# Kernel optimization log

Measured on AMD Instinct MI355X. Metric: run time of the kernel, lower is better.

The kernel has to match this reference:

```python
import jax, jax.numpy as jnp
import numpy as np

ALPHA = 0.2  # LeakyReLU negative slope
MASK_FILL = -9e15


def setup_inputs() -> dict:
    key = jax.random.key(0)
    k_x, k_adj, k_W, k_a = jax.random.split(key, 4)
    B, N, Fin, T, O = 8, 1024, 64, 8, 128
    x = jax.random.normal(k_x, (B, N, Fin, T), dtype=jnp.float32)
    adj = (jax.random.uniform(k_adj, (N, N)) < 0.05).astype(jnp.float32)
    adj = jnp.maximum(adj, jnp.eye(N, dtype=jnp.float32))
    W = jax.random.normal(k_W, (Fin, O), dtype=jnp.float32) * (1.414 * (6.0 / (Fin + O)) ** 0.5)
    a = jax.random.normal(k_a, (2 * O, 1), dtype=jnp.float32) * (1.414 * (6.0 / (2 * O + 1)) ** 0.5)
    return {"x": x, "adj": adj, "W": W, "a": a}


def reference(x, adj, W, a):
    # x: (B, N, Fin, T), adj: (N, N), W: (Fin, O), a: (2O, 1)
    O = W.shape[1]
    xt = jnp.transpose(x, (0, 3, 1, 2))                 # (B, T, N, Fin)
    Wh = jnp.einsum('btnf,fo->btno', xt, W)             # (B, T, N, O)
    a1 = a[:O, 0]                                       # (O,)
    a2 = a[O:, 0]                                       # (O,)
    Wh1 = Wh @ a1                                       # (B, T, N)
    Wh2 = Wh @ a2                                       # (B, T, N)
    e = Wh1[..., :, None] + Wh2[..., None, :]           # (B, T, N, N): e_ij = Wh1_i + Wh2_j
    e = jax.nn.leaky_relu(e, negative_slope=ALPHA)
    e = jnp.where(adj > 0, e, MASK_FILL)
    attn = jax.nn.softmax(e, axis=-1)                   # softmax over neighbors j (torch dim=1 on (N,N))
    # dropout on attention is identity at inference (training=False)
    h_prime = jnp.einsum('btij,btjo->btio', attn, Wh)   # (B, T, N, O)
    out = jnp.transpose(h_prime, (0, 2, 3, 1))          # (B, N, O, T)
    return jax.nn.elu(out)                              # concat=True -> ELU
```

## Files before the change

kernel.cpp:

```cpp
#include <hip/hip_runtime.h>
#include <math.h>
#include <stdint.h>

#define ALPHA 0.2f

typedef __attribute__((ext_vector_type(8)))  short bf16x8;
typedef __attribute__((ext_vector_type(4)))  float f32x4;
typedef __attribute__((ext_vector_type(16))) float f32x16;

__device__ __forceinline__ uint32_t pack_bf16(float a, float b) {
    return ((__float_as_uint(a) + 0x8000u) >> 16) |
           ((__float_as_uint(b) + 0x8000u) & 0xFFFF0000u);
}

__global__ __launch_bounds__(512) void k_wh(const float* __restrict__ x,
                                            const float* __restrict__ W,
                                            const float* __restrict__ a,
                                            uint4* __restrict__ Whf,
                                            float* __restrict__ Wh1,
                                            float* __restrict__ Wh2) {
    __shared__ float xs[16 * 512];
    __shared__ float Wv[128 * 68];

    const int tid = threadIdx.x;
    const int b   = blockIdx.x & 7;
    const int jt  = blockIdx.x >> 3;

    const float4* xg4 = (const float4*)(x + (size_t)(b * 1024 + jt * 16) * 512);
    #pragma unroll
    for (int i = 0; i < 4; ++i) {
        int    idx = tid + i * 512;
        float4 v   = xg4[idx];
        int jl  = idx >> 7;
        int rem = idx & 127;
        int f   = rem >> 1;
        int tq  = rem & 1;
        int kk  = f ^ ((jl >> 2) << 2);
        float* dst = &xs[jl * 512 + (tq * 4) * 64 + kk];
        dst[0]   = v.x;
        dst[64]  = v.y;
        dst[128] = v.z;
        dst[192] = v.w;
    }
    const float4* Wg4 = (const float4*)W;
    #pragma unroll
    for (int i = 0; i < 4; ++i) {
        int    idx = tid + i * 512;
        float4 v   = Wg4[idx];
        int k  = idx >> 5;
        int o0 = (idx & 31) * 4;
        #pragma unroll
        for (int c = 0; c < 4; ++c) {
            int o   = o0 + c;
            int adr = o * 68 + ((((k >> 2) ^ ((o >> 3) & 7)) << 2) | (k & 3));
            Wv[adr] = (&v.x)[c];
        }
    }
    __syncthreads();

    const int w  = tid >> 6;
    const int l  = tid & 63;
    const int q  = l >> 4;
    const int om = l & 15;
    const int t  = w;

    float acc[4][8];
    #pragma unroll
    for (int jj = 0; jj < 4; ++jj)
        #pragma unroll
        for (int nt = 0; nt < 8; ++nt) acc[jj][nt] = 0.f;

    for (int kc = 0; kc < 64; kc += 4) {
        float4 xv[4], wv[8];
        const int kx = kc ^ (q << 2);
        #pragma unroll
        for (int jj = 0; jj < 4; ++jj)
            xv[jj] = *(const float4*)&xs[(q * 4 + jj) * 512 + t * 64 + kx];
        #pragma unroll
        for (int nt = 0; nt < 8; ++nt) {
            int og  = nt * 16 + om;
            int grp = (kc >> 2) ^ ((nt * 2 + (om >> 3)) & 7);
            wv[nt]  = *(const float4*)&Wv[og * 68 + grp * 4];
        }
        #pragma unroll
        for (int jj = 0; jj < 4; ++jj) {
            #pragma unroll
            for (int nt = 0; nt < 8; ++nt) {
                float s = acc[jj][nt];
                s = fmaf(xv[jj].x, wv[nt].x, s);
                s = fmaf(xv[jj].y, wv[nt].y, s);
                s = fmaf(xv[jj].z, wv[nt].z, s);
                s = fmaf(xv[jj].w, wv[nt].w, s);
                acc[jj][nt] = s;
            }
        }
    }

    const int bt = b * 8 + t;

    float a1v[8], a2v[8];
    #pragma unroll
    for (int nt = 0; nt < 8; ++nt) {
        a1v[nt] = a[nt * 16 + om];
        a2v[nt] = a[128 + nt * 16 + om];
    }
    #pragma unroll
    for (int jj = 0; jj < 4; ++jj) {
        float s1 = 0.f, s2 = 0.f;
        #pragma unroll
        for (int nt = 0; nt < 8; ++nt) {
            s1 = fmaf(acc[jj][nt], a1v[nt], s1);
            s2 = fmaf(acc[jj][nt], a2v[nt], s2);
        }
        #pragma unroll
        for (int off = 1; off < 16; off <<= 1) {
            s1 += __shfl_xor(s1, off);
            s2 += __shfl_xor(s2, off);
        }
        if (om == 0) {
            int j = jt * 16 + q * 4 + jj;
            Wh1[bt * 1024 + j] = s1;
            Wh2[bt * 1024 + j] = s2;
        }
    }

    #pragma unroll
    for (int nt = 0; nt < 8; ++nt) {
        uint2 st;
        st.x = pack_bf16(acc[0][nt], acc[1][nt]);
        st.y = pack_bf16(acc[2][nt], acc[3][nt]);
        int    lane2 = ((q >> 1) << 5) | ((nt & 1) << 4) | om;
        size_t fidx  = ((size_t)(bt * 4 + (nt >> 1)) * 64 + jt) * 64 + lane2;
        char*  p     = (char*)(Whf + fidx) + ((q & 1) << 3);
        *(uint2*)p = st;
    }
}

__global__ __launch_bounds__(256) void k_adjb(const float* __restrict__ adj,
                                              unsigned char* __restrict__ adjq) {
    int idx = blockIdx.x * 256 + threadIdx.x;
    int i   = idx >> 7;
    int pos = idx & 127;
    const float4* a4 = (const float4*)adj + idx * 2;
    float4 v0 = a4[0], v1 = a4[1];
    unsigned int by = 0;
    by |= (v0.x > 0.f) ? 1u : 0u;
    by |= (v0.y > 0.f) ? 2u : 0u;
    by |= (v0.z > 0.f) ? 4u : 0u;
    by |= (v0.w > 0.f) ? 8u : 0u;
    by |= (v1.x > 0.f) ? 16u : 0u;
    by |= (v1.y > 0.f) ? 32u : 0u;
    by |= (v1.z > 0.f) ? 64u : 0u;
    by |= (v1.w > 0.f) ? 128u : 0u;
    adjq[(i << 7) + ((pos & 1) << 6) + (((pos >> 1) & 1) << 5) + (pos >> 2)] = (unsigned char)by;
}

__global__ __launch_bounds__(256) void k_agg(const uint4* __restrict__ Whf,
                                             const float* __restrict__ Wh1,
                                             const float* __restrict__ Wh2,
                                             const unsigned char* __restrict__ adjq,
                                             float* __restrict__ out) {
    __shared__ __attribute__((aligned(16))) uint4 bstage[2][2048];
    __shared__ __attribute__((aligned(16))) float efsE[1024];
    __shared__ __attribute__((aligned(16))) float efsF[1024];
    __shared__ float wh1s[128];
    __shared__ float m2s[4];

    const int tid   = threadIdx.x;
    const int b     = blockIdx.x & 7;
    const int t     = (blockIdx.x >> 3) & 7;
    const int itile = blockIdx.x >> 6;
    const int bt    = b * 8 + t;
    const int i0    = itile * 128;

    const int w   = tid >> 6;
    const int l   = tid & 63;
    const int col = l & 31;
    const int g   = l >> 5;
    const int row = w * 32 + col;

    const uint4* plane = Whf + (size_t)bt * 16384;

    uint4 pf[8];
    #pragma unroll
    for (int f = 0; f < 8; ++f) pf[f] = plane[(w * 64 + f) * 64 + l];

    const uint4* ap = (const uint4*)(adjq + ((size_t)(i0 + row) << 7) + (g << 6));
    uint4 am[4];
    #pragma unroll
    for (int f = 0; f < 4; ++f) am[f] = ap[f];

    const float* wh2g = Wh2 + bt * 1024;
    float mx = -1e30f;
    #pragma unroll
    for (int rep = 0; rep < 4; ++rep) {
        int   j  = tid + rep * 256;
        float h2 = wh2g[j];
        efsE[j] = __expf(h2);
        efsF[j] = __expf(ALPHA * h2);
        mx = fmaxf(mx, h2);
    }
    #pragma unroll
    for (int off = 1; off < 64; off <<= 1) mx = fmaxf(mx, __shfl_xor(mx, off));
    if (l == 0) m2s[w] = mx;
    if (tid < 128) wh1s[tid] = Wh1[bt * 1024 + i0 + tid];

    #pragma unroll
    for (int f = 0; f < 8; ++f) bstage[0][(w * 8 + f) * 64 + l] = pf[f];
    __syncthreads();

    const float M2 = fmaxf(fmaxf(m2s[0], m2s[1]), fmaxf(m2s[2], m2s[3]));
    const float h1 = wh1s[row];
    const float e0 = h1 + M2;
    const float mp = fmaxf(e0, ALPHA * e0);
    const float Af = __expf(h1 - mp);
    const float Bf = __expf(ALPHA * h1 - mp);

    f32x16 acc[4];
    #pragma unroll
    for (int nt2 = 0; nt2 < 4; ++nt2)
        #pragma unroll
        for (int r = 0; r < 16; ++r) acc[nt2][r] = 0.f;
    f32x16 accl;
    #pragma unroll
    for (int r = 0; r < 16; ++r) accl[r] = 0.f;

    bf16x8 ones;
    #pragma unroll
    for (int i = 0; i < 8; ++i) ones[i] = (short)0x3F80;

    #pragma unroll
    for (int u = 0; u < 8; ++u) {
        if (u + 1 < 8) {
            #pragma unroll
            for (int f = 0; f < 8; ++f)
                pf[f] = plane[(w * 64 + (u + 1) * 8 + f) * 64 + l];
        }

        #pragma unroll
        for (int ts = 0; ts < 8; ++ts) {
            const int jb = u * 128 + ts * 16 + g * 8;
            float4 E0 = *(const float4*)&efsE[jb];
            float4 E1 = *(const float4*)&efsE[jb + 4];
            float4 F0 = *(const float4*)&efsF[jb];
            float4 F1 = *(const float4*)&efsF[jb + 4];

            const int      pe = (ts & 1) * 32 + u * 4 + (ts >> 1);
            const uint4    av = am[pe >> 4];
            const int      cc = (pe >> 2) & 3;
            const uint32_t cw = (cc == 0) ? av.x : (cc == 1) ? av.y
                               : (cc == 2) ? av.z : av.w;
            const uint32_t by = (cw >> ((pe & 3) * 8)) & 0xFFu;

            float p[8];
            p[0] = fmaxf(Af * E0.x, Bf * F0.x) * (float)((by >> 0) & 1u);
            p[1] = fmaxf(Af * E0.y, Bf * F0.y) * (float)((by >> 1) & 1u);
            p[2] = fmaxf(Af * E0.z, Bf * F0.z) * (float)((by >> 2) & 1u);
            p[3] = fmaxf(Af * E0.w, Bf * F0.w) * (float)((by >> 3) & 1u);
            p[4] = fmaxf(Af * E1.x, Bf * F1.x) * (float)((by >> 4) & 1u);
            p[5] = fmaxf(Af * E1.y, Bf * F1.y) * (float)((by >> 5) & 1u);
            p[6] = fmaxf(Af * E1.z, Bf * F1.z) * (float)((by >> 6) & 1u);
            p[7] = fmaxf(Af * E1.w, Bf * F1.w) * (float)((by >> 7) & 1u);

            union { uint32_t u32[4]; bf16x8 v; } pk;
            #pragma unroll
            for (int r = 0; r < 4; ++r)
                pk.u32[r] = pack_bf16(p[2 * r], p[2 * r + 1]);

            #pragma unroll
            for (int nt2 = 0; nt2 < 4; ++nt2) {
                union { uint4 u4; bf16x8 v; } br;
                br.u4 = bstage[u & 1][(nt2 * 8 + ts) * 64 + l];
                acc[nt2] = __builtin_amdgcn_mfma_f32_32x32x16_bf16(
                    pk.v, br.v, acc[nt2], 0, 0, 0);
            }
            accl = __builtin_amdgcn_mfma_f32_32x32x16_bf16(
                pk.v, ones, accl, 0, 0, 0);
        }

        if (u + 1 < 8) {
            #pragma unroll
            for (int f = 0; f < 8; ++f)
                bstage[(u + 1) & 1][(w * 8 + f) * 64 + l] = pf[f];
        }
        __syncthreads();
    }

    float* og = out + ((size_t)(b * 1024 + i0 + w * 32)) * 1024 + t;
    #pragma unroll
    for (int reg = 0; reg < 16; ++reg) {
        const int   r    = (reg & 3) + 8 * (reg >> 2) + 4 * g;
        const float linv = 1.0f / accl[reg];
        #pragma unroll
        for (int nt2 = 0; nt2 < 4; ++nt2) {
            float v = acc[nt2][reg] * linv;
            v = v > 0.f ? v : __expf(v) - 1.f;
            og[(size_t)r * 1024 + (nt2 * 32 + col) * 8] = v;
        }
    }
}

extern "C" void kernel_launch(void* const* d_in, const int* in_sizes, int n_in,
                              void* d_out, int out_size, void* d_ws, size_t ws_size,
                              hipStream_t stream) {
    const float* x   = (const float*)d_in[0];
    const float* adj = (const float*)d_in[1];
    const float* W   = (const float*)d_in[2];
    const float* a   = (const float*)d_in[3];
    float* out = (float*)d_out;

    uint4*         Whf  = (uint4*)d_ws;
    float*         Wh1  = (float*)(Whf + 1048576);
    float*         Wh2  = Wh1 + 65536;
    unsigned char* adjq = (unsigned char*)(Wh2 + 65536);

    k_wh  <<<512, 512, 0, stream>>>(x, W, a, Whf, Wh1, Wh2);
    k_adjb<<<512, 256, 0, stream>>>(adj, adjq);
    k_agg <<<512, 256, 0, stream>>>(Whf, Wh1, Wh2, adjq, out);
}
```

Measured before the change: 145.4 us.

## Merge preprocessing kernels, async LDS staging, scalar row-sum, MFMA priority

The adjacency bit-packing kernel is folded into the Wh projection kernel as extra blocks, which saves one launch. In the aggregation kernel, Wh tiles are copied global-to-LDS with global_load_lds instead of passing through registers. The softmax denominator is now a per-thread scalar sum plus a shuffle rather than an extra MFMA against a ones vector. s_setprio is raised around the MFMA block. Risks: the double-buffered async LDS writes may need explicit vmcnt waits before the barrier. The row sum now uses fp32 p values while the numerator uses bf16-rounded ones, a small numeric mismatch.

```diff
diff --git a/kernel.cpp b/kernel.cpp
--- a/kernel.cpp
+++ b/kernel.cpp
@@ -5,7 +5,6 @@
 #define ALPHA 0.2f
 
 typedef __attribute__((ext_vector_type(8)))  short bf16x8;
-typedef __attribute__((ext_vector_type(4)))  float f32x4;
 typedef __attribute__((ext_vector_type(16))) float f32x16;
 
 __device__ __forceinline__ uint32_t pack_bf16(float a, float b) {
@@ -13,14 +12,43 @@
            ((__float_as_uint(b) + 0x8000u) & 0xFFFF0000u);
 }
 
-__global__ __launch_bounds__(512) void k_wh(const float* __restrict__ x,
-                                            const float* __restrict__ W,
-                                            const float* __restrict__ a,
-                                            uint4* __restrict__ Whf,
-                                            float* __restrict__ Wh1,
-                                            float* __restrict__ Wh2) {
+__device__ __forceinline__ void gload_lds16(const uint4* g, uint4* l) {
+    __builtin_amdgcn_global_load_lds(
+        (const __attribute__((address_space(1))) void*)g,
+        (__attribute__((address_space(3))) void*)l,
+        16, 0, 0);
+}
+
+__global__ __launch_bounds__(512) void k_pre(const float* __restrict__ x,
+                                             const float* __restrict__ W,
+                                             const float* __restrict__ a,
+                                             const float* __restrict__ adj,
+                                             uint4* __restrict__ Whf,
+                                             float* __restrict__ Wh1,
+                                             float* __restrict__ Wh2,
+                                             unsigned char* __restrict__ adjq) {
     __shared__ float xs[16 * 512];
     __shared__ float Wv[128 * 68];
+
+    if (blockIdx.x >= 512) {
+        int idx = (blockIdx.x - 512) * 512 + threadIdx.x;
+        int i   = idx >> 7;
+        int pos = idx & 127;
+        const float4* a4 = (const float4*)adj + idx * 2;
+        float4 v0 = a4[0], v1 = a4[1];
+        unsigned int by = 0;
+        by |= (v0.x > 0.f) ? 1u : 0u;
+        by |= (v0.y > 0.f) ? 2u : 0u;
+        by |= (v0.z > 0.f) ? 4u : 0u;
+        by |= (v0.w > 0.f) ? 8u : 0u;
+        by |= (v1.x > 0.f) ? 16u : 0u;
+        by |= (v1.y > 0.f) ? 32u : 0u;
+        by |= (v1.z > 0.f) ? 64u : 0u;
+        by |= (v1.w > 0.f) ? 128u : 0u;
+        adjq[(i << 7) + ((pos & 1) << 6) + (((pos >> 1) & 1) << 5) + (pos >> 2)] =
+            (unsigned char)by;
+        return;
+    }
 
     const int tid = threadIdx.x;
     const int b   = blockIdx.x & 7;
@@ -136,25 +164,6 @@
     }
 }
 
-__global__ __launch_bounds__(256) void k_adjb(const float* __restrict__ adj,
-                                              unsigned char* __restrict__ adjq) {
-    int idx = blockIdx.x * 256 + threadIdx.x;
-    int i   = idx >> 7;
-    int pos = idx & 127;
-    const float4* a4 = (const float4*)adj + idx * 2;
-    float4 v0 = a4[0], v1 = a4[1];
-    unsigned int by = 0;
-    by |= (v0.x > 0.f) ? 1u : 0u;
-    by |= (v0.y > 0.f) ? 2u : 0u;
-    by |= (v0.z > 0.f) ? 4u : 0u;
-    by |= (v0.w > 0.f) ? 8u : 0u;
-    by |= (v1.x > 0.f) ? 16u : 0u;
-    by |= (v1.y > 0.f) ? 32u : 0u;
-    by |= (v1.z > 0.f) ? 64u : 0u;
-    by |= (v1.w > 0.f) ? 128u : 0u;
-    adjq[(i << 7) + ((pos & 1) << 6) + (((pos >> 1) & 1) << 5) + (pos >> 2)] = (unsigned char)by;
-}
-
 __global__ __launch_bounds__(256) void k_agg(const uint4* __restrict__ Whf,
                                              const float* __restrict__ Wh1,
                                              const float* __restrict__ Wh2,
@@ -181,9 +190,9 @@
 
     const uint4* plane = Whf + (size_t)bt * 16384;
 
-    uint4 pf[8];
-    #pragma unroll
-    for (int f = 0; f < 8; ++f) pf[f] = plane[(w * 64 + f) * 64 + l];
+    #pragma unroll
+    for (int f = 0; f < 8; ++f)
+        gload_lds16(&plane[(w * 64 + f) * 64 + l], &bstage[0][(w * 8 + f) * 64]);
 
     const uint4* ap = (const uint4*)(adjq + ((size_t)(i0 + row) << 7) + (g << 6));
     uint4 am[4];
@@ -204,9 +213,6 @@
     for (int off = 1; off < 64; off <<= 1) mx = fmaxf(mx, __shfl_xor(mx, off));
     if (l == 0) m2s[w] = mx;
     if (tid < 128) wh1s[tid] = Wh1[bt * 1024 + i0 + tid];
-
-    #pragma unroll
-    for (int f = 0; f < 8; ++f) bstage[0][(w * 8 + f) * 64 + l] = pf[f];
     __syncthreads();
 
     const float M2 = fmaxf(fmaxf(m2s[0], m2s[1]), fmaxf(m2s[2], m2s[3]));
@@ -221,20 +227,15 @@
     for (int nt2 = 0; nt2 < 4; ++nt2)
         #pragma unroll
         for (int r = 0; r < 16; ++r) acc[nt2][r] = 0.f;
-    f32x16 accl;
-    #pragma unroll
-    for (int r = 0; r < 16; ++r) accl[r] = 0.f;
-
-    bf16x8 ones;
-    #pragma unroll
-    for (int i = 0; i < 8; ++i) ones[i] = (short)0x3F80;
+    float sacc = 0.f;
 
     #pragma unroll
     for (int u = 0; u < 8; ++u) {
         if (u + 1 < 8) {
             #pragma unroll
             for (int f = 0; f < 8; ++f)
-                pf[f] = plane[(w * 64 + (u + 1) * 8 + f) * 64 + l];
+                gload_lds16(&plane[(w * 64 + (u + 1) * 8 + f) * 64 + l],
+                            &bstage[(u + 1) & 1][(w * 8 + f) * 64]);
         }
 
         #pragma unroll
@@ -262,11 +263,15 @@
             p[6] = fmaxf(Af * E1.z, Bf * F1.z) * (float)((by >> 6) & 1u);
             p[7] = fmaxf(Af * E1.w, Bf * F1.w) * (float)((by >> 7) & 1u);
 
+            sacc += ((p[0] + p[1]) + (p[2] + p[3])) +
+                    ((p[4] + p[5]) + (p[6] + p[7]));
+
             union { uint32_t u32[4]; bf16x8 v; } pk;
             #pragma unroll
             for (int r = 0; r < 4; ++r)
                 pk.u32[r] = pack_bf16(p[2 * r], p[2 * r + 1]);
 
+            __builtin_amdgcn_s_setprio(1);
             #pragma unroll
             for (int nt2 = 0; nt2 < 4; ++nt2) {
                 union { uint4 u4; bf16x8 v; } br;
@@ -274,23 +279,19 @@
                 acc[nt2] = __builtin_amdgcn_mfma_f32_32x32x16_bf16(
                     pk.v, br.v, acc[nt2], 0, 0, 0);
             }
-            accl = __builtin_amdgcn_mfma_f32_32x32x16_bf16(
-                pk.v, ones, accl, 0, 0, 0);
-        }
-
-        if (u + 1 < 8) {
-            #pragma unroll
-            for (int f = 0; f < 8; ++f)
-                bstage[(u + 1) & 1][(w * 8 + f) * 64 + l] = pf[f];
-        }
+            __builtin_amdgcn_s_setprio(0);
+        }
+
         __syncthreads();
     }
+
+    float tot = sacc + __shfl_xor(sacc, 32);
 
     float* og = out + ((size_t)(b * 1024 + i0 + w * 32)) * 1024 + t;
     #pragma unroll
     for (int reg = 0; reg < 16; ++reg) {
         const int   r    = (reg & 3) + 8 * (reg >> 2) + 4 * g;
-        const float linv = 1.0f / accl[reg];
+        const float linv = 1.0f / __shfl(tot, r);
         #pragma unroll
         for (int nt2 = 0; nt2 < 4; ++nt2) {
             float v = acc[nt2][reg] * linv;
@@ -314,7 +315,6 @@
     float*         Wh2  = Wh1 + 65536;
     unsigned char* adjq = (unsigned char*)(Wh2 + 65536);
 
-    k_wh  <<<512, 512, 0, stream>>>(x, W, a, Whf, Wh1, Wh2);
-    k_adjb<<<512, 256, 0, stream>>>(adj, adjq);
-    k_agg <<<512, 256, 0, stream>>>(Whf, Wh1, Wh2, adjq, out);
-}
+    k_pre<<<768, 512, 0, stream>>>(x, W, a, adj, Whf, Wh1, Wh2, adjq);
+    k_agg<<<512, 256, 0, stream>>>(Whf, Wh1, Wh2, adjq, out);
+}
```

Result: slower. 192.5 us (+32.3%).
